# Optimization experiments

Hardware: AMD Instinct MI355X
Metric: run time of the kernel (lower is better)

## Reference

```python
import jax, jax.numpy as jnp
import numpy as np

EMB = 768
HEADS = 8

def setup_inputs() -> dict:
    key = jax.random.key(0)
    ks = jax.random.split(key, 5)
    x = jax.random.normal(ks[0], (8, 2048, EMB), dtype=jnp.float32)
    s = 1.0 / np.sqrt(EMB)
    W_qkv = jax.random.normal(ks[1], (EMB, 3 * EMB), dtype=jnp.float32) * s
    b_qkv = jnp.zeros((3 * EMB,), dtype=jnp.float32)
    W_proj = jax.random.normal(ks[2], (EMB, EMB), dtype=jnp.float32) * s
    b_proj = jnp.zeros((EMB,), dtype=jnp.float32)
    return {"x": x, "W_qkv": W_qkv, "b_qkv": b_qkv, "W_proj": W_proj, "b_proj": b_proj}

def reference(x, W_qkv, b_qkv, W_proj, b_proj):
    B, N, E = x.shape
    H = HEADS
    D = E // H
    qkv = x @ W_qkv + b_qkv  # [B, N, 3E]
    q, k, v = jnp.split(qkv, 3, axis=-1)
    # [B, N, E] -> [B, H, N, D]
    def heads(t):
        return t.reshape(B, N, H, D).transpose(0, 2, 1, 3)
    q, k, v = heads(q), heads(k), heads(v)
    # NOTE: original scales by 1/sqrt(emb_size), not 1/sqrt(head_dim)
    dots = jnp.einsum('bhnd,bhmd->bhnm', q, k) / jnp.sqrt(jnp.float32(E))
    attn = jax.nn.softmax(dots, axis=-1)  # dropout inactive (eval mode)
    out = jnp.einsum('bhnm,bhmd->bhnd', attn, v)
    out = out.transpose(0, 2, 1, 3).reshape(B, N, E)
    return out @ W_proj + b_proj
```

## Files before the change

kernel.cpp:

```cpp
#include <hip/hip_runtime.h>
#include <hip/hip_bf16.h>

typedef __attribute__((ext_vector_type(8))) short bf16x8;
typedef __attribute__((ext_vector_type(4))) short bf16x4;
typedef __attribute__((ext_vector_type(4))) float f32x4;
typedef __attribute__((ext_vector_type(16))) float f32x16;
typedef __attribute__((ext_vector_type(4))) unsigned int uint4v;

__device__ __forceinline__ short f2bf(float f) {
    unsigned int u = __float_as_uint(f);
    u += 0x7FFFu + ((u >> 16) & 1u);
    return (short)(u >> 16);
}

__device__ __forceinline__ unsigned cvtpk(float lo, float hi) {
    unsigned r;
    asm("v_cvt_pk_bf16_f32 %0, %1, %2" : "=v"(r) : "v"(lo), "v"(hi));
    return r;
}

__device__ __forceinline__ void gload_lds16(const void* g, void* l) {
    __builtin_amdgcn_global_load_lds(
        (const __attribute__((address_space(1))) void*)g,
        (__attribute__((address_space(3))) void*)l, 16, 0, 0);
}

__global__ __launch_bounds__(256) void cast_kernel(const float* __restrict__ in,
                                                   short* __restrict__ out, int n4) {
    int i = blockIdx.x * 256 + threadIdx.x;
    if (i >= n4) return;
    const f32x4 v = *(const f32x4*)(in + (size_t)i * 4);
    bf16x4 o;
    o[0] = f2bf(v[0]); o[1] = f2bf(v[1]); o[2] = f2bf(v[2]); o[3] = f2bf(v[3]);
    *(bf16x4*)(out + (size_t)i * 4) = o;
}

__global__ __launch_bounds__(256) void transpose_cast_kernel(const float* __restrict__ W,
                                                             short* __restrict__ WT,
                                                             int R, int C) {
    __shared__ float tile[64][65];
    const int bc = blockIdx.x * 64;
    const int br = blockIdx.y * 64;
    const int t = threadIdx.x;
#pragma unroll
    for (int i = 0; i < 16; ++i) {
        int o = t + 256 * i;
        int r = o >> 6, c = o & 63;
        tile[r][c] = W[(size_t)(br + r) * C + bc + c];
    }
    __syncthreads();
#pragma unroll
    for (int i = 0; i < 16; ++i) {
        int o = t + 256 * i;
        int c = o >> 6, r = o & 63;
        WT[(size_t)(bc + c) * R + br + r] = f2bf(tile[r][c]);
    }
}

__global__ __launch_bounds__(256, 3) void gemm1_kernel(
    const short* __restrict__ A, const short* __restrict__ BT,
    const float* __restrict__ bias,
    short* __restrict__ Qh, short* __restrict__ Kh, short* __restrict__ Vt)
{
    __shared__ short As[128][64];
    __shared__ short Bs[128][64];
    const int K = 768;
    const int t = threadIdx.x;
    const int w = t >> 6, l = t & 63;
    const int wr = w >> 1, wc = w & 1;
    const int lr = l & 15, lg = l >> 4;

    const int srow = w * 32 + (l >> 3);
    const int scol = (l & 7) * 8;
    const short* Ag = A + (size_t)blockIdx.x * 128 * K + (size_t)srow * K + scol;
    const short* Bg = BT + (size_t)blockIdx.y * 128 * K + (size_t)srow * K + scol;

    const f32x4 z4 = {0.f, 0.f, 0.f, 0.f};
    f32x4 acc[4][4];
#pragma unroll
    for (int i = 0; i < 4; ++i)
#pragma unroll
        for (int j = 0; j < 4; ++j) acc[i][j] = z4;

    for (int kt = 0; kt < K; kt += 64) {
#pragma unroll
        for (int i = 0; i < 4; ++i) {
            gload_lds16(Ag + kt + (size_t)(i * 8) * K, &As[w * 32 + i * 8][0]);
            gload_lds16(Bg + kt + (size_t)(i * 8) * K, &Bs[w * 32 + i * 8][0]);
        }
        __syncthreads();
#pragma unroll
        for (int kk = 0; kk < 2; ++kk) {
            bf16x8 af[4], bfr[4];
#pragma unroll
            for (int mi = 0; mi < 4; ++mi)
                af[mi] = *(const bf16x8*)&As[wr * 64 + mi * 16 + lr][kk * 32 + lg * 8];
#pragma unroll
            for (int ni = 0; ni < 4; ++ni)
                bfr[ni] = *(const bf16x8*)&Bs[wc * 64 + ni * 16 + lr][kk * 32 + lg * 8];
#pragma unroll
            for (int mi = 0; mi < 4; ++mi)
#pragma unroll
                for (int ni = 0; ni < 4; ++ni)
                    acc[mi][ni] = __builtin_amdgcn_mfma_f32_16x16x32_bf16(
                        af[mi], bfr[ni], acc[mi][ni], 0, 0, 0);
        }
        __syncthreads();
    }

    const float qs = 0.05205877f;
    const int rb = blockIdx.x * 128 + wr * 64;
    const int cb = blockIdx.y * 128 + wc * 64;
#pragma unroll
    for (int ni = 0; ni < 4; ++ni) {
        const int c = cb + ni * 16 + lr;
        const float bv = bias[c];
        const int which = (c >= 1536) ? 2 : (c >= 768 ? 1 : 0);
        const int cc = c - which * 768;
        const int h = cc / 96;
        const int d = cc - h * 96;
#pragma unroll
        for (int mi = 0; mi < 4; ++mi) {
            const int r0 = rb + mi * 16 + lg * 4;
            const int b = r0 >> 11, n0 = r0 & 2047;
            const int hb = b * 8 + h;
            if (which == 2) {
                bf16x4 pk;
#pragma unroll
                for (int r = 0; r < 4; ++r) pk[r] = f2bf(acc[mi][ni][r] + bv);
                const int ktile = n0 >> 6;
                const int s = (((n0 & 63) >> 3) ^ (d & 7));
                *(bf16x4*)&Vt[((size_t)(hb * 32 + ktile) * 96 + d) * 64 + s * 8 + (n0 & 7)] = pk;
            } else if (which == 1) {
#pragma unroll
                for (int r = 0; r < 4; ++r)
                    Kh[((size_t)hb * 2048 + n0 + r) * 104 + d] = f2bf(acc[mi][ni][r] + bv);
            } else {
#pragma unroll
                for (int r = 0; r < 4; ++r)
                    Qh[((size_t)hb * 2048 + n0 + r) * 96 + d] = f2bf((acc[mi][ni][r] + bv) * qs);
            }
        }
    }
}

__global__ __launch_bounds__(256, 3) void attn_kernel(
    const short* __restrict__ Qh, const short* __restrict__ Kh,
    const short* __restrict__ Vt, short* __restrict__ AO)
{
    __shared__ __align__(16) char smem[51200];
    short (*K0)[104] = (short (*)[104])smem;
    short (*K1)[104] = (short (*)[104])(smem + 13312);
    short* V0 = (short*)(smem + 26624);
    short* V1 = (short*)(smem + 38912);
    short (*Qs)[96] = (short (*)[96])smem;
    float (*ltab)[32] = (float (*)[32])smem;

    const int t = threadIdx.x;
    const int w = t >> 6, l = t & 63;
    const int ql = l & 31, hi = l >> 5;

    const unsigned L = blockIdx.y * 16 + blockIdx.x;
    const int bh = (int)((L & 7) + 8 * (L >> 7));
    const int qt = (int)((L >> 3) & 15);

    const short* Qg  = Qh + ((size_t)bh * 2048 + (size_t)qt * 128) * 96;
    const short* Kgp = Kh + (size_t)bh * 2048 * 104;
    const short* Vgt = Vt + (size_t)bh * 32 * 6144;

#pragma unroll
    for (int j = 0; j < 6; ++j) {
        const int idx = j * 4 + w;
        gload_lds16(Qg + idx * 512 + l * 8, smem + idx * 1024);
    }
    __syncthreads();
    bf16x8 qf[6];
#pragma unroll
    for (int kk = 0; kk < 6; ++kk)
        qf[kk] = *(const bf16x8*)&Qs[w * 32 + ql][kk * 16 + hi * 8];
    __syncthreads();

    auto stageK = [&](int kt, short (*wK)[104]) {
        const short* s = Kgp + kt * 6656 + l * 8;
#pragma unroll
        for (int j = 0; j < 4; ++j) {
            const int idx = j * 4 + w;
            if (idx < 13) gload_lds16(s + idx * 512, (char*)wK + idx * 1024);
        }
    };
    auto stageV = [&](int kt, short* wV) {
        const short* s = Vgt + kt * 6144 + l * 8;
#pragma unroll
        for (int j = 0; j < 3; ++j) {
            const int idx = j * 4 + w;
            gload_lds16(s + idx * 512, (char*)wV + idx * 1024);
        }
    };

    stageK(0, K0);
    stageV(0, V0);
    __syncthreads();

    f32x16 oacc[3];
#pragma unroll
    for (int i = 0; i < 3; ++i)
#pragma unroll
        for (int r = 0; r < 16; ++r) oacc[i][r] = 0.f;
    float lacc = 0.f;

    auto iter = [&](int kt, short (*rK)[104], const short* rV,
                    short (*wK)[104], short* wV) {
        if (kt < 31) { stageK(kt + 1, wK); stageV(kt + 1, wV); }

#pragma unroll
        for (int h = 0; h < 2; ++h) {
            f32x16 sa;
#pragma unroll
            for (int r = 0; r < 16; ++r) sa[r] = 0.f;
            __builtin_amdgcn_s_setprio(1);
#pragma unroll
            for (int kk = 0; kk < 6; ++kk) {
                bf16x8 kf = *(const bf16x8*)&rK[h * 32 + ql][kk * 16 + hi * 8];
                sa = __builtin_amdgcn_mfma_f32_32x32x16_bf16(kf, qf[kk], sa, 0, 0, 0);
            }
            __builtin_amdgcn_s_setprio(0);

            float p[16];
#pragma unroll
            for (int r = 0; r < 16; ++r) {
                p[r] = __builtin_amdgcn_exp2f(sa[r]);
                lacc += p[r];
            }
            unsigned x0 = cvtpk(p[0], p[1]),   y0 = cvtpk(p[4], p[5]);
            unsigned x1 = cvtpk(p[2], p[3]),   y1 = cvtpk(p[6], p[7]);
            unsigned x2 = cvtpk(p[8], p[9]),   y2 = cvtpk(p[12], p[13]);
            unsigned x3 = cvtpk(p[10], p[11]), y3 = cvtpk(p[14], p[15]);
            asm("v_permlane32_swap_b32 %0, %1" : "+v"(x0), "+v"(y0));
            asm("v_permlane32_swap_b32 %0, %1" : "+v"(x1), "+v"(y1));
            asm("v_permlane32_swap_b32 %0, %1" : "+v"(x2), "+v"(y2));
            asm("v_permlane32_swap_b32 %0, %1" : "+v"(x3), "+v"(y3));
            uint4v uA; uA[0] = x0; uA[1] = x1; uA[2] = y0; uA[3] = y1;
            uint4v uB; uB[0] = x2; uB[1] = x3; uB[2] = y2; uB[3] = y3;
            bf16x8 pa0 = __builtin_bit_cast(bf16x8, uA);
            bf16x8 pa1 = __builtin_bit_cast(bf16x8, uB);

            __builtin_amdgcn_s_setprio(1);
#pragma unroll
            for (int kb = 0; kb < 2; ++kb) {
                const int c = (h * 2 + kb) * 2 + hi;
                const bf16x8 paf = kb ? pa1 : pa0;
#pragma unroll
                for (int db = 0; db < 3; ++db) {
                    const int row = db * 32 + ql;
                    bf16x8 vf = *(const bf16x8*)&rV[row * 64 + ((c ^ (row & 7)) << 3)];
                    oacc[db] = __builtin_amdgcn_mfma_f32_32x32x16_bf16(paf, vf, oacc[db], 0, 0, 0);
                }
            }
            __builtin_amdgcn_s_setprio(0);
        }
        __syncthreads();
    };

    for (int kt = 0; kt < 32; kt += 2) {
        iter(kt,     K0, V0, K1, V1);
        iter(kt + 1, K1, V1, K0, V0);
    }

    float lsum = lacc + __shfl_xor(lacc, 32);
    if (l < 32) ltab[w][l] = lsum;
    asm volatile("s_waitcnt lgkmcnt(0)" ::: "memory");

    float linv[16];
#pragma unroll
    for (int r = 0; r < 16; ++r) {
        const int q = (r & 3) + 8 * (r >> 2) + 4 * hi;
        linv[r] = 1.0f / ltab[w][q];
    }

    const int b = bh >> 3, h2 = bh & 7;
    const size_t rowbase = (size_t)b * 2048 + qt * 128 + w * 32;
#pragma unroll
    for (int db = 0; db < 3; ++db) {
#pragma unroll
        for (int r = 0; r < 16; ++r) {
            const int q = (r & 3) + 8 * (r >> 2) + 4 * hi;
            AO[(rowbase + q) * 768 + h2 * 96 + db * 32 + ql] = f2bf(oacc[db][r] * linv[r]);
        }
    }
}

__global__ __launch_bounds__(256, 3) void gemm2_kernel(
    const short* __restrict__ A, const short* __restrict__ BT,
    const float* __restrict__ bias, float* __restrict__ out)
{
    __shared__ short As[128][64];
    __shared__ short Bs[128][64];
    const int K = 768;
    const int t = threadIdx.x;
    const int w = t >> 6, l = t & 63;
    const int wr = w >> 1, wc = w & 1;
    const int lr = l & 15, lg = l >> 4;

    const int srow = w * 32 + (l >> 3);
    const int scol = (l & 7) * 8;
    const short* Ag = A + (size_t)blockIdx.x * 128 * K + (size_t)srow * K + scol;
    const short* Bg = BT + (size_t)blockIdx.y * 128 * K + (size_t)srow * K + scol;

    const f32x4 z4 = {0.f, 0.f, 0.f, 0.f};
    f32x4 acc[4][4];
#pragma unroll
    for (int i = 0; i < 4; ++i)
#pragma unroll
        for (int j = 0; j < 4; ++j) acc[i][j] = z4;

    for (int kt = 0; kt < K; kt += 64) {
#pragma unroll
        for (int i = 0; i < 4; ++i) {
            gload_lds16(Ag + kt + (size_t)(i * 8) * K, &As[w * 32 + i * 8][0]);
            gload_lds16(Bg + kt + (size_t)(i * 8) * K, &Bs[w * 32 + i * 8][0]);
        }
        __syncthreads();
#pragma unroll
        for (int kk = 0; kk < 2; ++kk) {
            bf16x8 af[4], bfr[4];
#pragma unroll
            for (int mi = 0; mi < 4; ++mi)
                af[mi] = *(const bf16x8*)&As[wr * 64 + mi * 16 + lr][kk * 32 + lg * 8];
#pragma unroll
            for (int ni = 0; ni < 4; ++ni)
                bfr[ni] = *(const bf16x8*)&Bs[wc * 64 + ni * 16 + lr][kk * 32 + lg * 8];
#pragma unroll
            for (int mi = 0; mi < 4; ++mi)
#pragma unroll
                for (int ni = 0; ni < 4; ++ni)
                    acc[mi][ni] = __builtin_amdgcn_mfma_f32_16x16x32_bf16(
                        af[mi], bfr[ni], acc[mi][ni], 0, 0, 0);
        }
        __syncthreads();
    }

    const int rb = blockIdx.x * 128 + wr * 64;
    const int cb = blockIdx.y * 128 + wc * 64;
#pragma unroll
    for (int ni = 0; ni < 4; ++ni) {
        const int c = cb + ni * 16 + lr;
        const float bv = bias[c];
#pragma unroll
        for (int mi = 0; mi < 4; ++mi) {
            const int r0 = rb + mi * 16 + lg * 4;
#pragma unroll
            for (int r = 0; r < 4; ++r)
                out[(size_t)(r0 + r) * 768 + c] = acc[mi][ni][r] + bv;
        }
    }
}

extern "C" void kernel_launch(void* const* d_in, const int* in_sizes, int n_in,
                              void* d_out, int out_size, void* d_ws, size_t ws_size,
                              hipStream_t stream) {
    const float* x     = (const float*)d_in[0];
    const float* Wqkv  = (const float*)d_in[1];
    const float* bqkv  = (const float*)d_in[2];
    const float* Wproj = (const float*)d_in[3];
    const float* bproj = (const float*)d_in[4];
    float* out = (float*)d_out;

    char* ws = (char*)d_ws;
    short* xb     = (short*)(ws);
    short* WqkvT  = (short*)(ws + 25165824);
    short* WprojT = (short*)(ws + 28704768);
    short* Qh     = (short*)(ws + 29884416);
    short* Kh     = (short*)(ws + 55050240);
    short* Vt     = (short*)(ws + 82313216);
    short* AO     = xb;

    cast_kernel<<<12288, 256, 0, stream>>>(x, xb, 3145728);
    transpose_cast_kernel<<<dim3(36, 12), 256, 0, stream>>>(Wqkv, WqkvT, 768, 2304);
    transpose_cast_kernel<<<dim3(12, 12), 256, 0, stream>>>(Wproj, WprojT, 768, 768);
    gemm1_kernel<<<dim3(128, 18), 256, 0, stream>>>(xb, WqkvT, bqkv, Qh, Kh, Vt);
    attn_kernel<<<dim3(16, 64), 256, 0, stream>>>(Qh, Kh, Vt, AO);
    gemm2_kernel<<<dim3(128, 6), 256, 0, stream>>>(AO, WprojT, bproj, out);
}
```

Before: 239.5 us.

## Double attention query tile per wave, fuse prep kernels, raise GEMM occupancy

The attention kernel now gives each wave two 32-row query blocks (256 queries per block) that share every K and V fragment read from LDS. This halves K/V staging traffic per query and doubles the MFMA work per LDS read, at the cost of more registers and half as many blocks (launch bounds lowered to 1). The three preprocessing kernels (x cast and two weight transpose-casts) are merged into one launch to cut launch overhead. The GEMM launch-bound occupancy hints are raised from 3 to 4 waves.

```diff
diff --git a/kernel.cpp b/kernel.cpp
--- a/kernel.cpp
+++ b/kernel.cpp
@@ -25,23 +25,32 @@
         (__attribute__((address_space(3))) void*)l, 16, 0, 0);
 }
 
-__global__ __launch_bounds__(256) void cast_kernel(const float* __restrict__ in,
-                                                   short* __restrict__ out, int n4) {
-    int i = blockIdx.x * 256 + threadIdx.x;
-    if (i >= n4) return;
-    const f32x4 v = *(const f32x4*)(in + (size_t)i * 4);
-    bf16x4 o;
-    o[0] = f2bf(v[0]); o[1] = f2bf(v[1]); o[2] = f2bf(v[2]); o[3] = f2bf(v[3]);
-    *(bf16x4*)(out + (size_t)i * 4) = o;
-}
-
-__global__ __launch_bounds__(256) void transpose_cast_kernel(const float* __restrict__ W,
-                                                             short* __restrict__ WT,
-                                                             int R, int C) {
+__global__ __launch_bounds__(256) void prep_kernel(
+    const float* __restrict__ x, short* __restrict__ xb,
+    const float* __restrict__ Wqkv, short* __restrict__ WqkvT,
+    const float* __restrict__ Wproj, short* __restrict__ WprojT)
+{
     __shared__ float tile[64][65];
-    const int bc = blockIdx.x * 64;
-    const int br = blockIdx.y * 64;
     const int t = threadIdx.x;
+    const unsigned bx = blockIdx.x;
+    if (bx < 2048) {
+        size_t base = (size_t)bx * 256 + t;
+#pragma unroll
+        for (int it = 0; it < 6; ++it) {
+            size_t i = base + (size_t)it * 524288;
+            const f32x4 v = *(const f32x4*)(x + i * 4);
+            bf16x4 o;
+            o[0] = f2bf(v[0]); o[1] = f2bf(v[1]); o[2] = f2bf(v[2]); o[3] = f2bf(v[3]);
+            *(bf16x4*)(xb + i * 4) = o;
+        }
+        return;
+    }
+    const float* W; short* WT; int C, tiles_x, tt;
+    if (bx < 2480) { W = Wqkv;  WT = WqkvT;  C = 2304; tiles_x = 36; tt = (int)bx - 2048; }
+    else           { W = Wproj; WT = WprojT; C = 768;  tiles_x = 12; tt = (int)bx - 2480; }
+    const int R = 768;
+    const int bc = (tt % tiles_x) * 64;
+    const int br = (tt / tiles_x) * 64;
 #pragma unroll
     for (int i = 0; i < 16; ++i) {
         int o = t + 256 * i;
@@ -57,7 +66,7 @@
     }
 }
 
-__global__ __launch_bounds__(256, 3) void gemm1_kernel(
+__global__ __launch_bounds__(256, 4) void gemm1_kernel(
     const short* __restrict__ A, const short* __restrict__ BT,
     const float* __restrict__ bias,
     short* __restrict__ Qh, short* __restrict__ Kh, short* __restrict__ Vt)
@@ -144,7 +153,7 @@
     }
 }
 
-__global__ __launch_bounds__(256, 3) void attn_kernel(
+__global__ __launch_bounds__(256, 1) void attn_kernel(
     const short* __restrict__ Qh, const short* __restrict__ Kh,
     const short* __restrict__ Vt, short* __restrict__ AO)
 {
@@ -154,106 +163,116 @@
     short* V0 = (short*)(smem + 26624);
     short* V1 = (short*)(smem + 38912);
     short (*Qs)[96] = (short (*)[96])smem;
-    float (*ltab)[32] = (float (*)[32])smem;
+    float (*ltab)[64] = (float (*)[64])smem;
 
     const int t = threadIdx.x;
     const int w = t >> 6, l = t & 63;
     const int ql = l & 31, hi = l >> 5;
 
-    const unsigned L = blockIdx.y * 16 + blockIdx.x;
-    const int bh = (int)((L & 7) + 8 * (L >> 7));
-    const int qt = (int)((L >> 3) & 15);
-
-    const short* Qg  = Qh + ((size_t)bh * 2048 + (size_t)qt * 128) * 96;
+    const unsigned L = blockIdx.y * 8 + blockIdx.x;
+    const int bh = (int)((L & 7) + 8 * (L >> 6));
+    const int qt = (int)((L >> 3) & 7);
+
+    const short* Qg  = Qh + ((size_t)bh * 2048 + (size_t)qt * 256) * 96;
     const short* Kgp = Kh + (size_t)bh * 2048 * 104;
     const short* Vgt = Vt + (size_t)bh * 32 * 6144;
 
 #pragma unroll
-    for (int j = 0; j < 6; ++j) {
+    for (int j = 0; j < 12; ++j) {
         const int idx = j * 4 + w;
         gload_lds16(Qg + idx * 512 + l * 8, smem + idx * 1024);
     }
     __syncthreads();
-    bf16x8 qf[6];
-#pragma unroll
-    for (int kk = 0; kk < 6; ++kk)
-        qf[kk] = *(const bf16x8*)&Qs[w * 32 + ql][kk * 16 + hi * 8];
+    bf16x8 qfA[6], qfB[6];
+#pragma unroll
+    for (int kk = 0; kk < 6; ++kk) {
+        qfA[kk] = *(const bf16x8*)&Qs[w * 64 + ql][kk * 16 + hi * 8];
+        qfB[kk] = *(const bf16x8*)&Qs[w * 64 + 32 + ql][kk * 16 + hi * 8];
+    }
     __syncthreads();
 
-    auto stageK = [&](int kt, short (*wK)[104]) {
+    auto stageK = [&](int kt, char* wK) {
         const short* s = Kgp + kt * 6656 + l * 8;
 #pragma unroll
         for (int j = 0; j < 4; ++j) {
             const int idx = j * 4 + w;
-            if (idx < 13) gload_lds16(s + idx * 512, (char*)wK + idx * 1024);
+            if (idx < 13) gload_lds16(s + idx * 512, wK + idx * 1024);
         }
     };
-    auto stageV = [&](int kt, short* wV) {
+    auto stageV = [&](int kt, char* wV) {
         const short* s = Vgt + kt * 6144 + l * 8;
 #pragma unroll
         for (int j = 0; j < 3; ++j) {
             const int idx = j * 4 + w;
-            gload_lds16(s + idx * 512, (char*)wV + idx * 1024);
+            gload_lds16(s + idx * 512, wV + idx * 1024);
         }
     };
 
-    stageK(0, K0);
-    stageV(0, V0);
+    stageK(0, (char*)K0);
+    stageV(0, (char*)V0);
     __syncthreads();
 
-    f32x16 oacc[3];
+    f32x16 oaccA[3], oaccB[3];
 #pragma unroll
     for (int i = 0; i < 3; ++i)
 #pragma unroll
-        for (int r = 0; r < 16; ++r) oacc[i][r] = 0.f;
-    float lacc = 0.f;
-
-    auto iter = [&](int kt, short (*rK)[104], const short* rV,
-                    short (*wK)[104], short* wV) {
+        for (int r = 0; r < 16; ++r) { oaccA[i][r] = 0.f; oaccB[i][r] = 0.f; }
+    float laccA = 0.f, laccB = 0.f;
+
+    auto softmax_repack = [&](const f32x16& sa, float& lacc, bf16x8& o0, bf16x8& o1) {
+        float p[16];
+#pragma unroll
+        for (int r = 0; r < 16; ++r) {
+            p[r] = __builtin_amdgcn_exp2f(sa[r]);
+            lacc += p[r];
+        }
+        unsigned x0 = cvtpk(p[0], p[1]),   y0 = cvtpk(p[4], p[5]);
+        unsigned x1 = cvtpk(p[2], p[3]),   y1 = cvtpk(p[6], p[7]);
+        unsigned x2 = cvtpk(p[8], p[9]),   y2 = cvtpk(p[12], p[13]);
+        unsigned x3 = cvtpk(p[10], p[11]), y3 = cvtpk(p[14], p[15]);
+        asm("v_permlane32_swap_b32 %0, %1" : "+v"(x0), "+v"(y0));
+        asm("v_permlane32_swap_b32 %0, %1" : "+v"(x1), "+v"(y1));
+        asm("v_permlane32_swap_b32 %0, %1" : "+v"(x2), "+v"(y2));
+        asm("v_permlane32_swap_b32 %0, %1" : "+v"(x3), "+v"(y3));
+        uint4v uA; uA[0] = x0; uA[1] = x1; uA[2] = y0; uA[3] = y1;
+        uint4v uB; uB[0] = x2; uB[1] = x3; uB[2] = y2; uB[3] = y3;
+        o0 = __builtin_bit_cast(bf16x8, uA);
+        o1 = __builtin_bit_cast(bf16x8, uB);
+    };
+
+    auto iter = [&](int kt, short (*rK)[104], const short* rV, char* wK, char* wV) {
         if (kt < 31) { stageK(kt + 1, wK); stageV(kt + 1, wV); }
 
 #pragma unroll
         for (int h = 0; h < 2; ++h) {
-            f32x16 sa;
-#pragma unroll
-            for (int r = 0; r < 16; ++r) sa[r] = 0.f;
+            f32x16 saA, saB;
+#pragma unroll
+            for (int r = 0; r < 16; ++r) { saA[r] = 0.f; saB[r] = 0.f; }
             __builtin_amdgcn_s_setprio(1);
 #pragma unroll
             for (int kk = 0; kk < 6; ++kk) {
                 bf16x8 kf = *(const bf16x8*)&rK[h * 32 + ql][kk * 16 + hi * 8];
-                sa = __builtin_amdgcn_mfma_f32_32x32x16_bf16(kf, qf[kk], sa, 0, 0, 0);
+                saA = __builtin_amdgcn_mfma_f32_32x32x16_bf16(kf, qfA[kk], saA, 0, 0, 0);
+                saB = __builtin_amdgcn_mfma_f32_32x32x16_bf16(kf, qfB[kk], saB, 0, 0, 0);
             }
             __builtin_amdgcn_s_setprio(0);
 
-            float p[16];
-#pragma unroll
-            for (int r = 0; r < 16; ++r) {
-                p[r] = __builtin_amdgcn_exp2f(sa[r]);
-                lacc += p[r];
-            }
-            unsigned x0 = cvtpk(p[0], p[1]),   y0 = cvtpk(p[4], p[5]);
-            unsigned x1 = cvtpk(p[2], p[3]),   y1 = cvtpk(p[6], p[7]);
-            unsigned x2 = cvtpk(p[8], p[9]),   y2 = cvtpk(p[12], p[13]);
-            unsigned x3 = cvtpk(p[10], p[11]), y3 = cvtpk(p[14], p[15]);
-            asm("v_permlane32_swap_b32 %0, %1" : "+v"(x0), "+v"(y0));
-            asm("v_permlane32_swap_b32 %0, %1" : "+v"(x1), "+v"(y1));
-            asm("v_permlane32_swap_b32 %0, %1" : "+v"(x2), "+v"(y2));
-            asm("v_permlane32_swap_b32 %0, %1" : "+v"(x3), "+v"(y3));
-            uint4v uA; uA[0] = x0; uA[1] = x1; uA[2] = y0; uA[3] = y1;
-            uint4v uB; uB[0] = x2; uB[1] = x3; uB[2] = y2; uB[3] = y3;
-            bf16x8 pa0 = __builtin_bit_cast(bf16x8, uA);
-            bf16x8 pa1 = __builtin_bit_cast(bf16x8, uB);
+            bf16x8 paA0, paA1, paB0, paB1;
+            softmax_repack(saA, laccA, paA0, paA1);
+            softmax_repack(saB, laccB, paB0, paB1);
 
             __builtin_amdgcn_s_setprio(1);
 #pragma unroll
             for (int kb = 0; kb < 2; ++kb) {
                 const int c = (h * 2 + kb) * 2 + hi;
-                const bf16x8 paf = kb ? pa1 : pa0;
+                const bf16x8 pA = kb ? paA1 : paA0;
+                const bf16x8 pB = kb ? paB1 : paB0;
 #pragma unroll
                 for (int db = 0; db < 3; ++db) {
                     const int row = db * 32 + ql;
                     bf16x8 vf = *(const bf16x8*)&rV[row * 64 + ((c ^ (row & 7)) << 3)];
-                    oacc[db] = __builtin_amdgcn_mfma_f32_32x32x16_bf16(paf, vf, oacc[db], 0, 0, 0);
+                    oaccA[db] = __builtin_amdgcn_mfma_f32_32x32x16_bf16(pA, vf, oaccA[db], 0, 0, 0);
+                    oaccB[db] = __builtin_amdgcn_mfma_f32_32x32x16_bf16(pB, vf, oaccB[db], 0, 0, 0);
                 }
             }
             __builtin_amdgcn_s_setprio(0);
@@ -262,34 +281,32 @@
     };
 
     for (int kt = 0; kt < 32; kt += 2) {
-        iter(kt,     K0, V0, K1, V1);
-        iter(kt + 1, K1, V1, K0, V0);
-    }
-
-    float lsum = lacc + __shfl_xor(lacc, 32);
-    if (l < 32) ltab[w][l] = lsum;
+        iter(kt,     K0, V0, (char*)K1, (char*)V1);
+        iter(kt + 1, K1, V1, (char*)K0, (char*)V0);
+    }
+
+    float lsumA = laccA + __shfl_xor(laccA, 32);
+    float lsumB = laccB + __shfl_xor(laccB, 32);
+    if (hi == 0) ltab[w][ql] = lsumA;
+    else         ltab[w][32 + ql] = lsumB;
     asm volatile("s_waitcnt lgkmcnt(0)" ::: "memory");
 
-    float linv[16];
-#pragma unroll
-    for (int r = 0; r < 16; ++r) {
-        const int q = (r & 3) + 8 * (r >> 2) + 4 * hi;
-        linv[r] = 1.0f / ltab[w][q];
-    }
-
     const int b = bh >> 3, h2 = bh & 7;
-    const size_t rowbase = (size_t)b * 2048 + qt * 128 + w * 32;
+    const size_t rowbase = (size_t)b * 2048 + qt * 256 + w * 64;
 #pragma unroll
     for (int db = 0; db < 3; ++db) {
 #pragma unroll
         for (int r = 0; r < 16; ++r) {
-            const int q = (r & 3) + 8 * (r >> 2) + 4 * hi;
-            AO[(rowbase + q) * 768 + h2 * 96 + db * 32 + ql] = f2bf(oacc[db][r] * linv[r]);
-        }
-    }
-}
-
-__global__ __launch_bounds__(256, 3) void gemm2_kernel(
+            const int qr = (r & 3) + 8 * (r >> 2) + 4 * hi;
+            const float liA = 1.0f / ltab[w][qr];
+            const float liB = 1.0f / ltab[w][32 + qr];
+            AO[(rowbase + qr) * 768 + h2 * 96 + db * 32 + ql] = f2bf(oaccA[db][r] * liA);
+            AO[(rowbase + 32 + qr) * 768 + h2 * 96 + db * 32 + ql] = f2bf(oaccB[db][r] * liB);
+        }
+    }
+}
+
+__global__ __launch_bounds__(256, 4) void gemm2_kernel(
     const short* __restrict__ A, const short* __restrict__ BT,
     const float* __restrict__ bias, float* __restrict__ out)
 {
@@ -374,10 +391,8 @@
     short* Vt     = (short*)(ws + 82313216);
     short* AO     = xb;
 
-    cast_kernel<<<12288, 256, 0, stream>>>(x, xb, 3145728);
-    transpose_cast_kernel<<<dim3(36, 12), 256, 0, stream>>>(Wqkv, WqkvT, 768, 2304);
-    transpose_cast_kernel<<<dim3(12, 12), 256, 0, stream>>>(Wproj, WprojT, 768, 768);
+    prep_kernel<<<2624, 256, 0, stream>>>(x, xb, Wqkv, WqkvT, Wproj, WprojT);
     gemm1_kernel<<<dim3(128, 18), 256, 0, stream>>>(xb, WqkvT, bqkv, Qh, Kh, Vt);
-    attn_kernel<<<dim3(16, 64), 256, 0, stream>>>(Qh, Kh, Vt, AO);
+    attn_kernel<<<dim3(8, 64), 256, 0, stream>>>(Qh, Kh, Vt, AO);
     gemm2_kernel<<<dim3(128, 6), 256, 0, stream>>>(AO, WprojT, bproj, out);
 }
```

Result: slower. 254.6 us (+6.3%).
